# Performance work log

Hardware: AMD Instinct MI355X
Metric: run time of the kernel (lower is better)

The kernel has to match this reference:

```python
import jax, jax.numpy as jnp
import numpy as np

EMB = 1024
HEADS = 16
HEAD_DIM = EMB // HEADS
FF = 4 * EMB
EPS = 1e-5


def setup_inputs() -> dict:
    key = jax.random.key(0)
    ks = jax.random.split(key, 16)
    s = 0.02
    return {
        "x": jax.random.normal(ks[0], (2, 2048, EMB), dtype=jnp.float32),
        "ln1_g": jnp.ones((EMB,), jnp.float32),
        "ln1_b": jnp.zeros((EMB,), jnp.float32),
        "Wq": jax.random.normal(ks[1], (EMB, EMB), jnp.float32) * s,
        "bq": jnp.zeros((EMB,), jnp.float32),
        "Wk": jax.random.normal(ks[2], (EMB, EMB), jnp.float32) * s,
        "bk": jnp.zeros((EMB,), jnp.float32),
        "Wv": jax.random.normal(ks[3], (EMB, EMB), jnp.float32) * s,
        "bv": jnp.zeros((EMB,), jnp.float32),
        "Wo": jax.random.normal(ks[4], (EMB, EMB), jnp.float32) * s,
        "bo": jnp.zeros((EMB,), jnp.float32),
        "ln2_g": jnp.ones((EMB,), jnp.float32),
        "ln2_b": jnp.zeros((EMB,), jnp.float32),
        "W1": jax.random.normal(ks[5], (EMB, FF), jnp.float32) * s,
        "b1": jnp.zeros((FF,), jnp.float32),
        "W2": jax.random.normal(ks[6], (FF, EMB), jnp.float32) * s,
        "b2": jnp.zeros((EMB,), jnp.float32),
    }


def _layernorm(x, g, b):
    mu = jnp.mean(x, axis=-1, keepdims=True)
    var = jnp.var(x, axis=-1, keepdims=True)
    return (x - mu) * jax.lax.rsqrt(var + EPS) * g + b


def _attention(x, Wq, bq, Wk, bk, Wv, bv, Wo, bo):
    B, T, C = x.shape
    # [B,T,C] -> [B,H,T,Dh]
    def split(y):
        return y.reshape(B, T, HEADS, HEAD_DIM).transpose(0, 2, 1, 3)
    Q = split(x @ Wq + bq)
    K = split(x @ Wk + bk)
    V = split(x @ Wv + bv)
    att = jnp.einsum("bhqd,bhkd->bhqk", Q, K) / np.sqrt(HEAD_DIM).astype(np.float32)
    causal = jnp.tril(jnp.ones((T, T), bool))
    att = jnp.where(causal, att, -jnp.inf)
    att = jax.nn.softmax(att, axis=-1)
    out = jnp.einsum("bhqk,bhkd->bhqd", att, V)
    out = out.transpose(0, 2, 1, 3).reshape(B, T, C)
    return out @ Wo + bo


def reference(x, ln1_g, ln1_b, Wq, bq, Wk, bk, Wv, bv, Wo, bo,
              ln2_g, ln2_b, W1, b1, W2, b2):
    # dropout is identity in eval mode
    x = x + _attention(_layernorm(x, ln1_g, ln1_b), Wq, bq, Wk, bk, Wv, bv, Wo, bo)
    h = _layernorm(x, ln2_g, ln2_b)
    h = jax.nn.gelu(h @ W1 + b1, approximate=False) @ W2 + b2
    return x + h
```

## Files before the change

kernel.cpp:

```cpp
#include <hip/hip_runtime.h>
#include <hip/hip_bf16.h>

typedef __attribute__((ext_vector_type(4))) float f32x4;
typedef __attribute__((ext_vector_type(8))) short bf16x8;
typedef unsigned int u32;
typedef unsigned short u16;

#define GASP __attribute__((address_space(1)))
#define LASP __attribute__((address_space(3)))

__device__ __forceinline__ u16 f2bf(float f) {
  u32 u = __float_as_uint(f);
  return (u16)((u + 0x7fffu + ((u >> 16) & 1u)) >> 16);
}

__device__ __forceinline__ u32 cvtpk(float lo, float hi) {
  u32 r;
  asm("v_cvt_pk_bf16_f32 %0, %1, %2" : "=v"(r) : "v"(lo), "v"(hi));
  return r;
}

__device__ __forceinline__ void gl_lds16(const void* g, void* l) {
  __builtin_amdgcn_global_load_lds((const GASP u32*)g, (LASP u32*)l, 16, 0, 0);
}

struct CastArgs {
  const float* s[6];
  u16* d[6];
};

__global__ __launch_bounds__(256) void cast_w(CastArgs a) {
  int bid = blockIdx.x;
  int w, t, K, N, kshift;
  if (bid < 4096)      { w = bid >> 10; t = bid & 1023; K = 1024; N = 1024; kshift = 5; }
  else if (bid < 8192) { w = 4; t = bid - 4096; K = 1024; N = 4096; kshift = 5; }
  else                 { w = 5; t = bid - 8192; K = 4096; N = 1024; kshift = 7; }
  int tk = t & ((1 << kshift) - 1);
  int tn = t >> kshift;
  int k0 = tk << 5, n0 = tn << 5;
  const float* src = a.s[w];
  u16* dst = a.d[w];
  __shared__ u16 tile[32][36];
  int r = threadIdx.x >> 3, c0 = (threadIdx.x & 7) << 2;
  float4 v = *(const float4*)&src[(size_t)(k0 + r) * N + n0 + c0];
  tile[c0 + 0][r] = f2bf(v.x);
  tile[c0 + 1][r] = f2bf(v.y);
  tile[c0 + 2][r] = f2bf(v.z);
  tile[c0 + 3][r] = f2bf(v.w);
  __syncthreads();
  ushort4 o;
  o.x = tile[r][c0 + 0];
  o.y = tile[r][c0 + 1];
  o.z = tile[r][c0 + 2];
  o.w = tile[r][c0 + 3];
  *(ushort4*)&dst[(size_t)(n0 + r) * K + k0 + c0] = o;
}

__global__ __launch_bounds__(256) void ln_k(const float* __restrict__ x, const float* __restrict__ g,
                                            const float* __restrict__ b, u16* __restrict__ out) {
  int row = blockIdx.x;
  int tid = threadIdx.x;
  float4 v = *(const float4*)&x[(size_t)row * 1024 + tid * 4];
  float s = v.x + v.y + v.z + v.w;
  float ss = v.x * v.x + v.y * v.y + v.z * v.z + v.w * v.w;
#pragma unroll
  for (int o = 32; o >= 1; o >>= 1) {
    s += __shfl_xor(s, o, 64);
    ss += __shfl_xor(ss, o, 64);
  }
  __shared__ float red[8];
  int wv = tid >> 6;
  if ((tid & 63) == 0) { red[wv] = s; red[wv + 4] = ss; }
  __syncthreads();
  s = red[0] + red[1] + red[2] + red[3];
  ss = red[4] + red[5] + red[6] + red[7];
  float mu = s * (1.0f / 1024.0f);
  float var = ss * (1.0f / 1024.0f) - mu * mu;
  float rstd = rsqrtf(var + 1e-5f);
  float4 gv = *(const float4*)&g[tid * 4];
  float4 bv = *(const float4*)&b[tid * 4];
  ushort4 o4;
  o4.x = f2bf((v.x - mu) * rstd * gv.x + bv.x);
  o4.y = f2bf((v.y - mu) * rstd * gv.y + bv.y);
  o4.z = f2bf((v.z - mu) * rstd * gv.z + bv.z);
  o4.w = f2bf((v.w - mu) * rstd * gv.w + bv.w);
  *(ushort4*)&out[(size_t)row * 1024 + tid * 4] = o4;
}

template <int MODE>
__global__ __launch_bounds__(512, 2) void gemm_256(
    const u16* __restrict__ A, const u16* __restrict__ Bt,
    const float* __restrict__ bias0, const float* __restrict__ bias1, const float* __restrict__ bias2,
    void* outp, int nbx, int M, int N, int K) {
  __shared__ __align__(16) u16 As[3][256 * 32];
  __shared__ __align__(16) u16 Bs[3][256 * 32];
  const int tid = threadIdx.x;
  const int w = tid >> 6, lane = tid & 63;
  const int nwg = gridDim.x;
  const int cpx = nwg >> 3;
  const int sb = (blockIdx.x & 7) * cpx + (blockIdx.x >> 3);
  const int m0 = (sb / nbx) << 8, n0 = (sb % nbx) << 8;

  const u16* aS[2];
  const u16* bS[2];
  char* asB = (char*)As;
  char* bsB = (char*)Bs;
#pragma unroll
  for (int i = 0; i < 2; ++i) {
    int p = w * 2048 + i * 1024 + lane * 16;
    int r = p >> 6;
    int cl = ((p >> 4) & 3) ^ ((r >> 1) & 3);
    aS[i] = A + (size_t)(m0 + r) * K + cl * 8;
    bS[i] = Bt + (size_t)(n0 + r) * K + cl * 8;
  }
  f32x4 acc[8][4];
#pragma unroll
  for (int i = 0; i < 8; ++i)
#pragma unroll
    for (int j = 0; j < 4; ++j) acc[i][j] = f32x4{0.f, 0.f, 0.f, 0.f};

  const int wr = w >> 2, wc = w & 3;
  const int qi = lane & 15;
  int aOff[8], bOff[4];
#pragma unroll
  for (int mm = 0; mm < 8; ++mm) {
    int rowa = wr * 128 + mm * 16 + qi;
    aOff[mm] = rowa * 64 + (((lane >> 4) ^ ((rowa >> 1) & 3)) << 4);
  }
#pragma unroll
  for (int nn = 0; nn < 4; ++nn) {
    int rowb = wc * 64 + nn * 16 + qi;
    bOff[nn] = rowb * 64 + (((lane >> 4) ^ ((rowb >> 1) & 3)) << 4);
  }

  gl_lds16(aS[0], asB + w * 2048);
  gl_lds16(aS[1], asB + w * 2048 + 1024);
  gl_lds16(bS[0], bsB + w * 2048);
  gl_lds16(bS[1], bsB + w * 2048 + 1024);
  if (K > 32) {
    gl_lds16(aS[0] + 32, asB + 16384 + w * 2048);
    gl_lds16(aS[1] + 32, asB + 16384 + w * 2048 + 1024);
    gl_lds16(bS[0] + 32, bsB + 16384 + w * 2048);
    gl_lds16(bS[1] + 32, bsB + 16384 + w * 2048 + 1024);
  }
  int buf = 0;
  for (int ks = 0; ks < K; ks += 32) {
    if (ks + 32 >= K) { asm volatile("s_waitcnt vmcnt(0)" ::: "memory"); }
    else              { asm volatile("s_waitcnt vmcnt(4)" ::: "memory"); }
    __builtin_amdgcn_s_barrier();
    asm volatile("" ::: "memory");
    if (ks + 64 < K) {
      const int nb = ((buf + 2) % 3) * 16384;
      gl_lds16(aS[0] + ks + 64, asB + nb + w * 2048);
      gl_lds16(aS[1] + ks + 64, asB + nb + w * 2048 + 1024);
      gl_lds16(bS[0] + ks + 64, bsB + nb + w * 2048);
      gl_lds16(bS[1] + ks + 64, bsB + nb + w * 2048 + 1024);
    }
    const int tb = buf * 16384;
    bf16x8 av[8], bv[4];
#pragma unroll
    for (int mm = 0; mm < 8; ++mm) av[mm] = *(const bf16x8*)(asB + tb + aOff[mm]);
#pragma unroll
    for (int nn = 0; nn < 4; ++nn) bv[nn] = *(const bf16x8*)(bsB + tb + bOff[nn]);
    __builtin_amdgcn_s_setprio(1);
#pragma unroll
    for (int mm = 0; mm < 8; ++mm)
#pragma unroll
      for (int nn = 0; nn < 4; ++nn)
        acc[mm][nn] = __builtin_amdgcn_mfma_f32_16x16x32_bf16(av[mm], bv[nn], acc[mm][nn], 0, 0, 0);
    __builtin_amdgcn_s_setprio(0);
    buf = buf + 1;
    if (buf == 3) buf = 0;
  }

  const int g = lane >> 4, ci = lane & 15;
#pragma unroll
  for (int mm = 0; mm < 8; ++mm) {
#pragma unroll
    for (int nn = 0; nn < 4; ++nn) {
      int colb = n0 + wc * 64 + nn * 16 + ci;
      int rowbase = m0 + wr * 128 + mm * 16 + 4 * g;
      f32x4 c = acc[mm][nn];
      if constexpr (MODE == 2) {
        int sel = colb >> 10;
        int cc = colb & 1023;
        const float* bp = sel == 0 ? bias0 : (sel == 1 ? bias1 : bias2);
        float bb = bp[cc];
        int h = cc >> 6, d = cc & 63;
        int b_ = rowbase >> 11, tt = rowbase & 2047;
        if (sel == 2) {
          u16* op = (u16*)outp + 2ull * (4096ull * 1024ull);
          ushort4 o4;
          o4.x = f2bf(c[0] + bb);
          o4.y = f2bf(c[1] + bb);
          o4.z = f2bf(c[2] + bb);
          o4.w = f2bf(c[3] + bb);
          *(ushort4*)&op[((size_t)(b_ * 16 + h) * 64 + d) * 2048 + tt] = o4;
        } else {
          float scale = (sel == 0) ? 0.125f : 1.0f;
          u16* op = (u16*)outp + (size_t)sel * (4096ull * 1024ull);
#pragma unroll
          for (int r = 0; r < 4; ++r)
            op[((size_t)(b_ * 16 + h) * 2048 + tt + r) * 64 + d] = f2bf((c[r] + bb) * scale);
        }
      } else {
        float bb = bias0[colb];
#pragma unroll
        for (int r = 0; r < 4; ++r) {
          float v = c[r] + bb;
          float gl = 0.5f * v * (1.0f + erff(v * 0.70710678118654752f));
          ((u16*)outp)[(size_t)(rowbase + r) * N + colb] = f2bf(gl);
        }
      }
    }
  }
}

__global__ __launch_bounds__(512) void gemm_sk(
    const u16* __restrict__ A, const u16* __restrict__ Bt,
    const float* __restrict__ bias0, float* __restrict__ outp,
    const float* __restrict__ res, int M, int N, int K) {
  __shared__ __align__(16) union SM {
    struct { u16 As[2][3][128 * 32]; u16 Bs[2][3][128 * 32]; } t;
    float red[16][4][4][64];
  } sm;
  const int tid = threadIdx.x;
  const int w8 = tid >> 6, lane = tid & 63;
  const int gg = w8 >> 2, wl = w8 & 3;
  const int m0 = blockIdx.y << 7, n0 = blockIdx.x << 7;

  char* asB = (char*)sm.t.As[gg];
  char* bsB = (char*)sm.t.Bs[gg];
  const u16* aS[2];
  const u16* bS[2];
#pragma unroll
  for (int i = 0; i < 2; ++i) {
    int p = wl * 2048 + i * 1024 + lane * 16;
    int r = p >> 6;
    int cl = ((p >> 4) & 3) ^ ((r >> 1) & 3);
    aS[i] = A + (size_t)(m0 + r) * K + gg * 32 + cl * 8;
    bS[i] = Bt + (size_t)(n0 + r) * K + gg * 32 + cl * 8;
  }
  f32x4 acc[4][4];
#pragma unroll
  for (int i = 0; i < 4; ++i)
#pragma unroll
    for (int j = 0; j < 4; ++j) acc[i][j] = f32x4{0.f, 0.f, 0.f, 0.f};

  const int wr = wl >> 1, wc = wl & 1;
  int aOff[4], bOff[4];
#pragma unroll
  for (int mm = 0; mm < 4; ++mm) {
    int rowa = wr * 64 + mm * 16 + (lane & 15);
    aOff[mm] = rowa * 64 + (((lane >> 4) ^ ((rowa >> 1) & 3)) << 4);
    int rowb = wc * 64 + mm * 16 + (lane & 15);
    bOff[mm] = rowb * 64 + (((lane >> 4) ^ ((rowb >> 1) & 3)) << 4);
  }

  gl_lds16(aS[0], asB + wl * 2048);
  gl_lds16(aS[1], asB + wl * 2048 + 1024);
  gl_lds16(bS[0], bsB + wl * 2048);
  gl_lds16(bS[1], bsB + wl * 2048 + 1024);
  if (K > 64) {
    gl_lds16(aS[0] + 64, asB + 8192 + wl * 2048);
    gl_lds16(aS[1] + 64, asB + 8192 + wl * 2048 + 1024);
    gl_lds16(bS[0] + 64, bsB + 8192 + wl * 2048);
    gl_lds16(bS[1] + 64, bsB + 8192 + wl * 2048 + 1024);
  }
  int buf = 0;
  for (int ks = 0; ks < K; ks += 64) {
    if (ks + 64 >= K) { asm volatile("s_waitcnt vmcnt(0)" ::: "memory"); }
    else              { asm volatile("s_waitcnt vmcnt(4)" ::: "memory"); }
    __builtin_amdgcn_s_barrier();
    asm volatile("" ::: "memory");
    if (ks + 128 < K) {
      const int nb = ((buf + 2) % 3) * 8192;
      gl_lds16(aS[0] + ks + 128, asB + nb + wl * 2048);
      gl_lds16(aS[1] + ks + 128, asB + nb + wl * 2048 + 1024);
      gl_lds16(bS[0] + ks + 128, bsB + nb + wl * 2048);
      gl_lds16(bS[1] + ks + 128, bsB + nb + wl * 2048 + 1024);
    }
    const int tb = buf * 8192;
    bf16x8 av[4], bv[4];
#pragma unroll
    for (int mm = 0; mm < 4; ++mm) av[mm] = *(const bf16x8*)(asB + tb + aOff[mm]);
#pragma unroll
    for (int nn = 0; nn < 4; ++nn) bv[nn] = *(const bf16x8*)(bsB + tb + bOff[nn]);
#pragma unroll
    for (int mm = 0; mm < 4; ++mm)
#pragma unroll
      for (int nn = 0; nn < 4; ++nn)
        acc[mm][nn] = __builtin_amdgcn_mfma_f32_16x16x32_bf16(av[mm], bv[nn], acc[mm][nn], 0, 0, 0);
    buf = buf + 1;
    if (buf == 3) buf = 0;
  }

  __syncthreads();
  if (gg == 1) {
#pragma unroll
    for (int mm = 0; mm < 4; ++mm)
#pragma unroll
      for (int nn = 0; nn < 4; ++nn)
#pragma unroll
        for (int r = 0; r < 4; ++r) sm.red[mm * 4 + nn][r][wl][lane] = acc[mm][nn][r];
  }
  __syncthreads();
  if (gg == 0) {
    const int g = lane >> 4, ci = lane & 15;
#pragma unroll
    for (int mm = 0; mm < 4; ++mm) {
#pragma unroll
      for (int nn = 0; nn < 4; ++nn) {
        int colb = n0 + wc * 64 + nn * 16 + ci;
        int rowbase = m0 + wr * 64 + mm * 16 + 4 * g;
        float bb = bias0[colb];
#pragma unroll
        for (int r = 0; r < 4; ++r) {
          size_t idx = (size_t)(rowbase + r) * N + colb;
          outp[idx] = acc[mm][nn][r] + sm.red[mm * 4 + nn][r][wl][lane] + bb + res[idx];
        }
      }
    }
  }
}

__global__ __launch_bounds__(512) void attn_k(const u16* __restrict__ Q, const u16* __restrict__ Kg,
                                              const u16* __restrict__ Vt, u16* __restrict__ O) {
  __shared__ __align__(16) u16 Ks[2][64 * 64];
  __shared__ __align__(16) u16 Vs[2][64 * 64];
  const int bx = blockIdx.x;
  const int bh = blockIdx.y;
  const int tid = threadIdx.x, w = tid >> 6, lane = tid & 63;
  const int g = lane >> 4, qi = lane & 15;
  const u16* Qb = Q + (size_t)bh * 2048 * 64;
  const u16* Kb = Kg + (size_t)bh * 2048 * 64;
  const u16* Vtb = Vt + (size_t)bh * 64 * 2048;

  const int rS = tid >> 3, cS = tid & 7;
  const int csw = (cS ^ (rS & 7)) * 8;
  const u16* srcK = Kb + (size_t)rS * 64 + csw;
  const u16* srcV = Vtb + (size_t)rS * 2048 + csw;
  char* ksB = (char*)Ks;
  char* vsB = (char*)Vs;
  const int dstOff = tid * 16;

  int koff[4][2], voff[4][2];
#pragma unroll
  for (int t = 0; t < 4; ++t) {
    int row = 16 * t + qi;
#pragma unroll
    for (int h = 0; h < 2; ++h) koff[t][h] = row * 128 + (((4 * h + g) ^ (qi & 7)) << 4);
#pragma unroll
    for (int kt = 0; kt < 2; ++kt) voff[t][kt] = row * 128 + (((4 * kt + g) ^ (qi & 7)) << 4);
  }

  const int b_ = bh >> 4, hh = bh & 15;
  u32* Ou = (u32*)O;

  for (int job = 0; job < 2; ++job) {
    const int qt = job ? bx : 15 - bx;
    const int qrow = qt * 128 + w * 16 + qi;
    const int qmaxw = qt * 128 + w * 16 + 15;

    bf16x8 qf[2];
#pragma unroll
    for (int h = 0; h < 2; ++h)
      qf[h] = *(const bf16x8*)(Qb + (size_t)qrow * 64 + h * 32 + g * 8);

    f32x4 acc[4];
#pragma unroll
    for (int dt = 0; dt < 4; ++dt) acc[dt] = f32x4{0.f, 0.f, 0.f, 0.f};
    float m = -1e30f, lsum = 0.0f;

    __syncthreads();
    gl_lds16(srcK, ksB + dstOff);
    gl_lds16(srcV, vsB + dstOff);

    const int nsteps = 2 * qt + 2;
    int buf = 0;
    for (int s = 0; s < nsteps; ++s) {
      __syncthreads();
      if (s + 1 < nsteps) {
        int nb = buf ^ 1;
        gl_lds16(srcK + (size_t)(s + 1) * 4096, ksB + nb * 8192 + dstOff);
        gl_lds16(srcV + (size_t)(s + 1) * 64, vsB + nb * 8192 + dstOff);
      }
      const int kv0 = s * 64;
      if (kv0 <= qmaxw) {
        const int tb = buf * 8192;
        f32x4 st[4];
        __builtin_amdgcn_s_setprio(1);
#pragma unroll
        for (int t = 0; t < 4; ++t) {
          st[t] = f32x4{0.f, 0.f, 0.f, 0.f};
#pragma unroll
          for (int h = 0; h < 2; ++h) {
            bf16x8 kf = *(const bf16x8*)(ksB + tb + koff[t][h]);
            st[t] = __builtin_amdgcn_mfma_f32_16x16x32_bf16(kf, qf[h], st[t], 0, 0, 0);
          }
        }
        __builtin_amdgcn_s_setprio(0);
        float pvv[4][4];
        float tmax = -1e30f;
        if (kv0 + 63 > qmaxw) {
#pragma unroll
          for (int t = 0; t < 4; ++t)
#pragma unroll
            for (int r = 0; r < 4; ++r) {
              int key = kv0 + 16 * t + 4 * g + r;
              float sv = st[t][r];
              sv = (key <= qrow) ? sv : -1e30f;
              pvv[t][r] = sv;
              tmax = fmaxf(tmax, sv);
            }
        } else {
#pragma unroll
          for (int t = 0; t < 4; ++t)
#pragma unroll
            for (int r = 0; r < 4; ++r) {
              float sv = st[t][r];
              pvv[t][r] = sv;
              tmax = fmaxf(tmax, sv);
            }
        }
        tmax = fmaxf(tmax, __shfl_xor(tmax, 16, 64));
        tmax = fmaxf(tmax, __shfl_xor(tmax, 32, 64));
        if (!__all(tmax <= m + 8.0f)) {
          float mn = fmaxf(m, tmax);
          float corr = __expf(m - mn);
          lsum *= corr;
#pragma unroll
          for (int dt = 0; dt < 4; ++dt)
#pragma unroll
            for (int r = 0; r < 4; ++r) acc[dt][r] *= corr;
          m = mn;
        }
        float tsum = 0.f;
#pragma unroll
        for (int t = 0; t < 4; ++t)
#pragma unroll
          for (int r = 0; r < 4; ++r) {
            float e = __expf(pvv[t][r] - m);
            pvv[t][r] = e;
            tsum += e;
          }
        tsum += __shfl_xor(tsum, 16, 64);
        tsum += __shfl_xor(tsum, 32, 64);
        lsum += tsum;
        u32 pk[4][2], ex[4][2];
#pragma unroll
        for (int t = 0; t < 4; ++t)
#pragma unroll
          for (int p = 0; p < 2; ++p) {
            u32 v = cvtpk(pvv[t][2 * p], pvv[t][2 * p + 1]);
            pk[t][p] = v;
            ex[t][p] = (u32)__shfl_xor((int)v, 16, 64);
          }
        const bool ge = (g & 1) == 0;
        const bool G0 = (g >> 1) == 0;
        const bool innr = (g == 0) || (g == 3);
        u32 mm_[4][4];
#pragma unroll
        for (int t = 0; t < 4; ++t) {
          mm_[t][0] = ge ? pk[t][0] : ex[t][0];
          mm_[t][1] = ge ? pk[t][1] : ex[t][1];
          mm_[t][2] = ge ? ex[t][0] : pk[t][0];
          mm_[t][3] = ge ? ex[t][1] : pk[t][1];
        }
        union Frag { u32 u[4]; bf16x8 v; } f0, f1;
#pragma unroll
        for (int i = 0; i < 4; ++i) {
          u32 sel0 = G0 ? mm_[1][i] : mm_[0][i];
          u32 sel1 = G0 ? mm_[3][i] : mm_[2][i];
          u32 sw0 = (u32)__shfl_xor((int)sel0, 32, 64);
          u32 sw1 = (u32)__shfl_xor((int)sel1, 32, 64);
          u32 own0 = G0 ? mm_[0][i] : mm_[1][i];
          u32 own1 = G0 ? mm_[2][i] : mm_[3][i];
          f0.u[i] = innr ? own0 : sw0;
          f1.u[i] = innr ? own1 : sw1;
        }
        __builtin_amdgcn_s_setprio(1);
#pragma unroll
        for (int dt = 0; dt < 4; ++dt) {
          bf16x8 vfa = *(const bf16x8*)(vsB + tb + voff[dt][0]);
          acc[dt] = __builtin_amdgcn_mfma_f32_16x16x32_bf16(vfa, f0.v, acc[dt], 0, 0, 0);
          bf16x8 vfb = *(const bf16x8*)(vsB + tb + voff[dt][1]);
          acc[dt] = __builtin_amdgcn_mfma_f32_16x16x32_bf16(vfb, f1.v, acc[dt], 0, 0, 0);
        }
        __builtin_amdgcn_s_setprio(0);
      }
      buf ^= 1;
    }

    float rl = 1.0f / lsum;
    size_t rowq = (size_t)(b_ * 2048 + qrow);
#pragma unroll
    for (int dt = 0; dt < 4; ++dt) {
#pragma unroll
      for (int rp = 0; rp < 2; ++rp) {
        u32 pkd = cvtpk(acc[dt][rp * 2] * rl, acc[dt][rp * 2 + 1] * rl);
        size_t off = rowq * 1024 + hh * 64 + dt * 16 + 4 * g + rp * 2;
        Ou[off >> 1] = pkd;
      }
    }
  }
}

extern "C" void kernel_launch(void* const* d_in, const int* in_sizes, int n_in,
                              void* d_out, int out_size, void* d_ws, size_t ws_size,
                              hipStream_t stream) {
  const float* x    = (const float*)d_in[0];
  const float* ln1g = (const float*)d_in[1];
  const float* ln1b = (const float*)d_in[2];
  const float* Wq   = (const float*)d_in[3];
  const float* bq   = (const float*)d_in[4];
  const float* Wk   = (const float*)d_in[5];
  const float* bk   = (const float*)d_in[6];
  const float* Wv   = (const float*)d_in[7];
  const float* bv   = (const float*)d_in[8];
  const float* Wo   = (const float*)d_in[9];
  const float* bo   = (const float*)d_in[10];
  const float* ln2g = (const float*)d_in[11];
  const float* ln2b = (const float*)d_in[12];
  const float* W1   = (const float*)d_in[13];
  const float* b1   = (const float*)d_in[14];
  const float* W2   = (const float*)d_in[15];
  const float* b2   = (const float*)d_in[16];

  char* ws = (char*)d_ws;
  const size_t MB = 1ull << 20;
  u16* WqT = (u16*)(ws + 0 * MB);
  u16* WkT = (u16*)(ws + 2 * MB);
  u16* WvT = (u16*)(ws + 4 * MB);
  u16* WoT = (u16*)(ws + 6 * MB);
  u16* W1T = (u16*)(ws + 8 * MB);
  u16* W2T = (u16*)(ws + 16 * MB);
  u16* XN  = (u16*)(ws + 24 * MB);
  u16* Qb  = (u16*)(ws + 32 * MB);
  u16* Kb  = (u16*)(ws + 40 * MB);
  u16* Vtb = (u16*)(ws + 48 * MB);
  u16* Ob  = (u16*)(ws + 56 * MB);
  u16* Gb  = (u16*)(ws + 32 * MB);

  CastArgs ca;
  ca.s[0] = Wq; ca.s[1] = Wk; ca.s[2] = Wv; ca.s[3] = Wo; ca.s[4] = W1; ca.s[5] = W2;
  ca.d[0] = WqT; ca.d[1] = WkT; ca.d[2] = WvT; ca.d[3] = WoT; ca.d[4] = W1T; ca.d[5] = W2T;
  cast_w<<<12288, 256, 0, stream>>>(ca);

  ln_k<<<4096, 256, 0, stream>>>(x, ln1g, ln1b, XN);

  gemm_256<2><<<12 * 16, 512, 0, stream>>>(XN, WqT, bq, bk, bv, Qb, 12, 4096, 3072, 1024);

  attn_k<<<dim3(8, 32), 512, 0, stream>>>(Qb, Kb, Vtb, Ob);

  gemm_sk<<<dim3(8, 32), 512, 0, stream>>>(Ob, WoT, bo, (float*)d_out, x, 4096, 1024, 1024);

  ln_k<<<4096, 256, 0, stream>>>((const float*)d_out, ln2g, ln2b, XN);

  gemm_256<3><<<16 * 16, 512, 0, stream>>>(XN, W1T, b1, nullptr, nullptr, Gb, 16, 4096, 4096, 1024);

  gemm_sk<<<dim3(8, 32), 512, 0, stream>>>(Gb, W2T, b2, (float*)d_out, (const float*)d_out, 4096, 1024, 4096);
}
```

Baseline: 252.1 us.

## Deepen GEMM LDS pipelines to four stages and simplify attention softmax rescale

Both GEMM kernels move from a three-buffer to a four-buffer LDS ring, prefetching three k-tiles ahead, with waitcnt thresholds adjusted to the number of tiles remaining. The goal is to hide more global-load latency, at the cost of more LDS per workgroup, which could lower occupancy. In the attention kernel, the conditional lazy max-rescale is replaced by an unconditional rescale every tile. The inline v_cvt_pk_bf16_f32 asm is also replaced by software bf16 rounding, which adds ALU work in the softmax and output paths.

```diff
diff --git a/kernel.cpp b/kernel.cpp
--- a/kernel.cpp
+++ b/kernel.cpp
@@ -12,12 +12,6 @@
 __device__ __forceinline__ u16 f2bf(float f) {
   u32 u = __float_as_uint(f);
   return (u16)((u + 0x7fffu + ((u >> 16) & 1u)) >> 16);
-}
-
-__device__ __forceinline__ u32 cvtpk(float lo, float hi) {
-  u32 r;
-  asm("v_cvt_pk_bf16_f32 %0, %1, %2" : "=v"(r) : "v"(lo), "v"(hi));
-  return r;
 }
 
 __device__ __forceinline__ void gl_lds16(const void* g, void* l) {
@@ -92,8 +86,8 @@
     const u16* __restrict__ A, const u16* __restrict__ Bt,
     const float* __restrict__ bias0, const float* __restrict__ bias1, const float* __restrict__ bias2,
     void* outp, int nbx, int M, int N, int K) {
-  __shared__ __align__(16) u16 As[3][256 * 32];
-  __shared__ __align__(16) u16 Bs[3][256 * 32];
+  __shared__ __align__(16) u16 As[4][256 * 32];
+  __shared__ __align__(16) u16 Bs[4][256 * 32];
   const int tid = threadIdx.x;
   const int w = tid >> 6, lane = tid & 63;
   const int nwg = gridDim.x;
@@ -143,18 +137,26 @@
     gl_lds16(bS[0] + 32, bsB + 16384 + w * 2048);
     gl_lds16(bS[1] + 32, bsB + 16384 + w * 2048 + 1024);
   }
+  if (K > 64) {
+    gl_lds16(aS[0] + 64, asB + 32768 + w * 2048);
+    gl_lds16(aS[1] + 64, asB + 32768 + w * 2048 + 1024);
+    gl_lds16(bS[0] + 64, bsB + 32768 + w * 2048);
+    gl_lds16(bS[1] + 64, bsB + 32768 + w * 2048 + 1024);
+  }
   int buf = 0;
   for (int ks = 0; ks < K; ks += 32) {
-    if (ks + 32 >= K) { asm volatile("s_waitcnt vmcnt(0)" ::: "memory"); }
-    else              { asm volatile("s_waitcnt vmcnt(4)" ::: "memory"); }
+    const int rem = ((K - ks) >> 5) - 1;
+    if (rem >= 2)      { asm volatile("s_waitcnt vmcnt(8)" ::: "memory"); }
+    else if (rem == 1) { asm volatile("s_waitcnt vmcnt(4)" ::: "memory"); }
+    else               { asm volatile("s_waitcnt vmcnt(0)" ::: "memory"); }
     __builtin_amdgcn_s_barrier();
     asm volatile("" ::: "memory");
-    if (ks + 64 < K) {
-      const int nb = ((buf + 2) % 3) * 16384;
-      gl_lds16(aS[0] + ks + 64, asB + nb + w * 2048);
-      gl_lds16(aS[1] + ks + 64, asB + nb + w * 2048 + 1024);
-      gl_lds16(bS[0] + ks + 64, bsB + nb + w * 2048);
-      gl_lds16(bS[1] + ks + 64, bsB + nb + w * 2048 + 1024);
+    if (ks + 96 < K) {
+      const int nb = ((buf + 3) & 3) * 16384;
+      gl_lds16(aS[0] + ks + 96, asB + nb + w * 2048);
+      gl_lds16(aS[1] + ks + 96, asB + nb + w * 2048 + 1024);
+      gl_lds16(bS[0] + ks + 96, bsB + nb + w * 2048);
+      gl_lds16(bS[1] + ks + 96, bsB + nb + w * 2048 + 1024);
     }
     const int tb = buf * 16384;
     bf16x8 av[8], bv[4];
@@ -169,8 +171,7 @@
       for (int nn = 0; nn < 4; ++nn)
         acc[mm][nn] = __builtin_amdgcn_mfma_f32_16x16x32_bf16(av[mm], bv[nn], acc[mm][nn], 0, 0, 0);
     __builtin_amdgcn_s_setprio(0);
-    buf = buf + 1;
-    if (buf == 3) buf = 0;
+    buf = (buf + 1) & 3;
   }
 
   const int g = lane >> 4, ci = lane & 15;
@@ -221,7 +222,7 @@
     const float* __restrict__ bias0, float* __restrict__ outp,
     const float* __restrict__ res, int M, int N, int K) {
   __shared__ __align__(16) union SM {
-    struct { u16 As[2][3][128 * 32]; u16 Bs[2][3][128 * 32]; } t;
+    struct { u16 As[2][4][128 * 32]; u16 Bs[2][4][128 * 32]; } t;
     float red[16][4][4][64];
   } sm;
   const int tid = threadIdx.x;
@@ -267,18 +268,26 @@
     gl_lds16(bS[0] + 64, bsB + 8192 + wl * 2048);
     gl_lds16(bS[1] + 64, bsB + 8192 + wl * 2048 + 1024);
   }
+  if (K > 128) {
+    gl_lds16(aS[0] + 128, asB + 16384 + wl * 2048);
+    gl_lds16(aS[1] + 128, asB + 16384 + wl * 2048 + 1024);
+    gl_lds16(bS[0] + 128, bsB + 16384 + wl * 2048);
+    gl_lds16(bS[1] + 128, bsB + 16384 + wl * 2048 + 1024);
+  }
   int buf = 0;
   for (int ks = 0; ks < K; ks += 64) {
-    if (ks + 64 >= K) { asm volatile("s_waitcnt vmcnt(0)" ::: "memory"); }
-    else              { asm volatile("s_waitcnt vmcnt(4)" ::: "memory"); }
+    const int rem = ((K - ks) >> 6) - 1;
+    if (rem >= 2)      { asm volatile("s_waitcnt vmcnt(8)" ::: "memory"); }
+    else if (rem == 1) { asm volatile("s_waitcnt vmcnt(4)" ::: "memory"); }
+    else               { asm volatile("s_waitcnt vmcnt(0)" ::: "memory"); }
     __builtin_amdgcn_s_barrier();
     asm volatile("" ::: "memory");
-    if (ks + 128 < K) {
-      const int nb = ((buf + 2) % 3) * 8192;
-      gl_lds16(aS[0] + ks + 128, asB + nb + wl * 2048);
-      gl_lds16(aS[1] + ks + 128, asB + nb + wl * 2048 + 1024);
-      gl_lds16(bS[0] + ks + 128, bsB + nb + wl * 2048);
-      gl_lds16(bS[1] + ks + 128, bsB + nb + wl * 2048 + 1024);
+    if (ks + 192 < K) {
+      const int nb = ((buf + 3) & 3) * 8192;
+      gl_lds16(aS[0] + ks + 192, asB + nb + wl * 2048);
+      gl_lds16(aS[1] + ks + 192, asB + nb + wl * 2048 + 1024);
+      gl_lds16(bS[0] + ks + 192, bsB + nb + wl * 2048);
+      gl_lds16(bS[1] + ks + 192, bsB + nb + wl * 2048 + 1024);
     }
     const int tb = buf * 8192;
     bf16x8 av[4], bv[4];
@@ -291,8 +300,7 @@
 #pragma unroll
       for (int nn = 0; nn < 4; ++nn)
         acc[mm][nn] = __builtin_amdgcn_mfma_f32_16x16x32_bf16(av[mm], bv[nn], acc[mm][nn], 0, 0, 0);
-    buf = buf + 1;
-    if (buf == 3) buf = 0;
+    buf = (buf + 1) & 3;
   }
 
   __syncthreads();
@@ -425,34 +433,31 @@
         }
         tmax = fmaxf(tmax, __shfl_xor(tmax, 16, 64));
         tmax = fmaxf(tmax, __shfl_xor(tmax, 32, 64));
-        if (!__all(tmax <= m + 8.0f)) {
-          float mn = fmaxf(m, tmax);
-          float corr = __expf(m - mn);
-          lsum *= corr;
-#pragma unroll
-          for (int dt = 0; dt < 4; ++dt)
-#pragma unroll
-            for (int r = 0; r < 4; ++r) acc[dt][r] *= corr;
-          m = mn;
-        }
+        float mn = fmaxf(m, tmax);
+        float corr = __expf(m - mn);
         float tsum = 0.f;
 #pragma unroll
         for (int t = 0; t < 4; ++t)
 #pragma unroll
           for (int r = 0; r < 4; ++r) {
-            float e = __expf(pvv[t][r] - m);
+            float e = __expf(pvv[t][r] - mn);
             pvv[t][r] = e;
             tsum += e;
           }
         tsum += __shfl_xor(tsum, 16, 64);
         tsum += __shfl_xor(tsum, 32, 64);
-        lsum += tsum;
+        lsum = lsum * corr + tsum;
+        m = mn;
+#pragma unroll
+        for (int dt = 0; dt < 4; ++dt)
+#pragma unroll
+          for (int r = 0; r < 4; ++r) acc[dt][r] *= corr;
         u32 pk[4][2], ex[4][2];
 #pragma unroll
         for (int t = 0; t < 4; ++t)
 #pragma unroll
           for (int p = 0; p < 2; ++p) {
-            u32 v = cvtpk(pvv[t][2 * p], pvv[t][2 * p + 1]);
+            u32 v = (u32)f2bf(pvv[t][2 * p]) | ((u32)f2bf(pvv[t][2 * p + 1]) << 16);
             pk[t][p] = v;
             ex[t][p] = (u32)__shfl_xor((int)v, 16, 64);
           }
@@ -498,7 +503,9 @@
     for (int dt = 0; dt < 4; ++dt) {
 #pragma unroll
       for (int rp = 0; rp < 2; ++rp) {
-        u32 pkd = cvtpk(acc[dt][rp * 2] * rl, acc[dt][rp * 2 + 1] * rl);
+        u16 lo = f2bf(acc[dt][rp * 2] * rl);
+        u16 hi = f2bf(acc[dt][rp * 2 + 1] * rl);
+        u32 pkd = (u32)lo | ((u32)hi << 16);
         size_t off = rowq * 1024 + hh * 64 + dt * 16 + 4 * g + rp * 2;
         Ou[off >> 1] = pkd;
       }
```

New measurement: 258.4 us. 1.02x slower.
